# Kernel optimization log

Measured on AMD Instinct MI355X. Metric: run time of the kernel, lower is better.

Reference implementation:

```python
import jax, jax.numpy as jnp
import numpy as np

B, V, L = 2, 12000, 16
IN_F = 479  # 3+3+3+9+3+10+64+256(imgf)+128(gar_latent)


def setup_inputs() -> dict:
    key = jax.random.key(0)
    ks = jax.random.split(key, 12)

    def w(k, shape, fan_in):
        return (jax.random.normal(k, shape, jnp.float32) / np.sqrt(fan_in)).astype(jnp.float32)

    return {
        "x": jax.random.normal(ks[0], (B, V, IN_F), jnp.float32),
        "spiral_idx": jax.random.randint(ks[1], (V + 1, L), 0, V + 1),  # indices incl. dummy vertex V
        "W_point": w(ks[2], (IN_F, 256), IN_F),                 # pointMLP Linear, no bias
        "res1_W": w(ks[3], (2, 256 * L, 256), 256 * L),          # two SpiralConv(256,256)
        "res1_b": jnp.zeros((2, 256), jnp.float32),
        "W_mid": w(ks[4], (256, 128), 256),                      # midDown, no bias
        "ress_W": w(ks[5], (3, 2, 128 * L, 128), 128 * L),       # 3 residual blocks of SpiralConv(128,128)
        "ress_b": jnp.zeros((3, 2, 128), jnp.float32),
        "Wo1": w(ks[6], (512, 256), 512), "bo1": jnp.zeros((256,), jnp.float32),
        "Wo2": w(ks[7], (256, 128), 256), "bo2": jnp.zeros((128,), jnp.float32),
        "Wo3": w(ks[8], (128, 3), 128),  "bo3": jnp.zeros((3,), jnp.float32),
    }


def _spiral_conv(x, idx, Wc, bc, zp):
    # x: [B, Vp, C]; idx: [Vp, L] -> gather spiral neighborhoods then linear, mask dummy vertex
    Bn, Vp, C = x.shape
    g = x[:, idx.reshape(-1), :].reshape(Bn, Vp, -1)  # [B, Vp, L*C]
    return (g @ Wc + bc) * zp


def _res_block(x, idx, Wb, bb, zp):
    h = jax.nn.relu(_spiral_conv(x, idx, Wb[0], bb[0], zp))
    h = _spiral_conv(h, idx, Wb[1], bb[1], zp)
    return jax.nn.relu(h + x)


def reference(x, spiral_idx, W_point, res1_W, res1_b, W_mid, ress_W, ress_b,
              Wo1, bo1, Wo2, bo2, Wo3, bo3):
    pf = jax.nn.relu(x @ W_point)                                  # [B, V, 256]
    Bn = pf.shape[0]
    pfs = jnp.concatenate([pf, jnp.zeros((Bn, 1, pf.shape[-1]), pf.dtype)], axis=1)  # [B, V+1, 256]
    Vp = pfs.shape[1]
    zp = jnp.ones((1, Vp, 1), pf.dtype).at[0, -1, 0].set(0.0)       # zero_padding mask
    fs = (_res_block(pfs, spiral_idx, res1_W, res1_b, zp) @ W_mid) * zp  # [B, Vp, 128]
    gfs = jnp.max(fs[:, :-1, :], axis=1, keepdims=True)             # masked global max-pool [B,1,128]
    for i in range(3):
        fs = _res_block(fs, spiral_idx, ress_W[i], ress_b[i], zp)
    g = jnp.broadcast_to(gfs, (Bn, Vp, gfs.shape[-1])) * zp
    h = jnp.concatenate([pfs, fs, g], axis=-1)                      # [B, Vp, 512]
    h = jax.nn.relu(h @ Wo1 + bo1)
    h = jax.nn.relu(h @ Wo2 + bo2)
    out = h @ Wo3 + bo3
    return out[:, :-1, :]                                           # drop dummy vertex
```

## Files before the change

### kernel.cpp

```cpp
#include <hip/hip_runtime.h>
#include <cstdint>
#include <cfloat>
#include <cstddef>

constexpr int BATCH  = 2;
constexpr int V      = 12000;
constexpr int VP     = V + 1;
constexpr int M_ROWS = BATCH * VP;
constexpr int L_SP   = 16;

typedef _Float16 half_t;
typedef _Float16 half8 __attribute__((ext_vector_type(8)));
typedef float floatx4 __attribute__((ext_vector_type(4)));

__device__ __forceinline__ void async_cp16(const void* g, void* l) {
    __builtin_amdgcn_global_load_lds(
        (const __attribute__((address_space(1))) unsigned int*)g,
        (__attribute__((address_space(3))) unsigned int*)l, 16, 0, 0);
}

template<bool GATHER, int BM, int LGC>
__global__ __launch_bounds__(256, 4)
void gemm_mfma(const half_t* __restrict__ A, const half_t* __restrict__ Wt,
               const float* __restrict__ bias, const half_t* __restrict__ res,
               const int* __restrict__ idx, half_t* __restrict__ out,
               int M, int N, int K, int KA, int relu, int mask)
{
    constexpr int AF = BM / 32;
    __shared__ half_t As[BM * 64];
    __shared__ half_t Bs[64 * 64];

    const int tid  = threadIdx.x;
    const int lane = tid & 63;
    const int w    = tid >> 6;
    const int bm   = blockIdx.x, bn = blockIdx.y;

    const int goff = (((lane & 7) ^ ((lane >> 3) & 7)) << 3);
    const int rsub = lane >> 3;

    const int nB0 = bn * 64 + (w << 3) + rsub;
    const half_t* wp0 = Wt + (size_t)nB0 * K + goff;
    const half_t* wp1 = Wt + (size_t)(nB0 + 32) * K + goff;
    half_t* lB0 = &Bs[(size_t)((w << 6) + lane) * 8];
    half_t* lB1 = &Bs[(size_t)(((w + 4) << 6) + lane) * 8];

    int bb[AF], vv[AF];
    const half_t* aP[AF];
    half_t* lA[AF];
#pragma unroll
    for (int ai = 0; ai < AF; ++ai) {
        const int blk = w + (ai << 2);
        int m = bm * BM + (blk << 3) + rsub;
        if (m >= M) m = M - 1;
        bb[ai] = m / VP; vv[ai] = m - bb[ai] * VP;
        aP[ai] = GATHER ? nullptr : (A + (size_t)m * KA + goff);
        lA[ai] = &As[(size_t)((blk << 6) + lane) * 8];
    }

    const int wm = (w >> 1) * (BM / 2);
    const int wn = (w & 1) << 5;
    const int fr = lane & 15;
    const int q  = lane >> 4;
    const int f7 = fr & 7;

    floatx4 acc[AF][2] = {};

    int curl = -1;
    const half_t* gp[AF];
    const int Cm1 = (1 << LGC) - 1;

    const int nk = K >> 6;
    for (int t = 0; t < nk; ++t) {
        const int k0 = t << 6;
        if (GATHER) {
            const int l = k0 >> LGC;
            if (l != curl) {
                curl = l;
#pragma unroll
                for (int ai = 0; ai < AF; ++ai) {
                    const int j = idx[(vv[ai] << 4) + l];
                    gp[ai] = A + (((size_t)(bb[ai] * VP + j)) << LGC) + goff;
                }
            }
            const int ko = k0 & Cm1;
#pragma unroll
            for (int ai = 0; ai < AF; ++ai) async_cp16(gp[ai] + ko, lA[ai]);
        } else {
#pragma unroll
            for (int ai = 0; ai < AF; ++ai) async_cp16(aP[ai] + k0, lA[ai]);
        }
        async_cp16(wp0 + k0, lB0);
        async_cp16(wp1 + k0, lB1);
        __syncthreads();

#pragma unroll
        for (int s = 0; s < 2; ++s) {
            const int ck = ((((s << 2) | q) ^ f7) << 3);
            half8 af[AF], bf[2];
#pragma unroll
            for (int i = 0; i < AF; ++i)
                af[i] = *(const half8*)&As[(wm + (i << 4) + fr) * 64 + ck];
#pragma unroll
            for (int j = 0; j < 2; ++j)
                bf[j] = *(const half8*)&Bs[(wn + (j << 4) + fr) * 64 + ck];
#pragma unroll
            for (int i = 0; i < AF; ++i)
#pragma unroll
                for (int j = 0; j < 2; ++j)
                    acc[i][j] = __builtin_amdgcn_mfma_f32_16x16x32_f16(af[i], bf[j], acc[i][j], 0, 0, 0);
        }
        __syncthreads();
    }

    const int er = q << 2;
#pragma unroll
    for (int i = 0; i < AF; ++i) {
#pragma unroll
        for (int j = 0; j < 2; ++j) {
            const int n = bn * 64 + wn + (j << 4) + fr;
            const floatx4 a = acc[i][j];
#pragma unroll
            for (int r = 0; r < 4; ++r) {
                const int m = bm * BM + wm + (i << 4) + er + r;
                if (m >= M) continue;
                float val = a[r];
                if (bias) val += bias[n];
                if (res)  val += (float)res[(size_t)m * N + n];
                if (relu) val = fmaxf(val, 0.f);
                const int vvm = m - (m / VP) * VP;
                if (mask && vvm == VP - 1) val = 0.f;
                out[(size_t)m * N + n] = (half_t)val;
            }
        }
    }
}

__global__ void wcvt(const float* __restrict__ in, half_t* __restrict__ out,
                     int K, int N, int Kpad)
{
    __shared__ float t[32][33];
    const size_t ioff = (size_t)blockIdx.z * K * N;
    const size_t ooff = (size_t)blockIdx.z * N * Kpad;
    const int k0 = blockIdx.x * 32, n0 = blockIdx.y * 32;
    const int tx = threadIdx.x & 31, ty = threadIdx.x >> 5;
#pragma unroll
    for (int r = 0; r < 4; ++r) {
        const int k = k0 + ty + r * 8;
        t[ty + r * 8][tx] = (k < K && n0 + tx < N) ? in[ioff + (size_t)k * N + n0 + tx] : 0.f;
    }
    __syncthreads();
#pragma unroll
    for (int r = 0; r < 4; ++r) {
        const int n = n0 + ty + r * 8;
        const int k = k0 + tx;
        if (n < N && k < Kpad) out[ooff + (size_t)n * Kpad + k] = (half_t)t[tx][ty + r * 8];
    }
}

__global__ void cvt_x(const float* __restrict__ x, half_t* __restrict__ xh)
{
    const int m = blockIdx.x;
    const int b = m / VP, v = m - b * VP;
    for (int k = threadIdx.x; k < 512; k += 256) {
        float val = (v < V && k < 479) ? x[((size_t)b * V + v) * 479 + k] : 0.f;
        xh[(size_t)m * 512 + k] = (half_t)val;
    }
}

__global__ void maxpool1(const half_t* __restrict__ fs, float* __restrict__ pmax)
{
    const int b = blockIdx.x, chunk = blockIdx.y;
    const int c = threadIdx.x;
    const int v0 = chunk * (V / 32);
    float m = -FLT_MAX;
    const half_t* p = fs + ((size_t)b * VP + v0) * 128 + c;
    for (int v = 0; v < V / 32; ++v) { m = fmaxf(m, (float)*p); p += 128; }
    pmax[((size_t)b * 32 + chunk) * 128 + c] = m;
}
__global__ void maxpool2(const float* __restrict__ pmax, half_t* __restrict__ gfs)
{
    const int b = blockIdx.x, c = threadIdx.x;
    float m = -FLT_MAX;
    for (int i = 0; i < 32; ++i) m = fmaxf(m, pmax[((size_t)b * 32 + i) * 128 + c]);
    gfs[b * 128 + c] = (half_t)m;
}

__global__ void concat_k(const half_t* __restrict__ pfs, const half_t* __restrict__ fs,
                         const half_t* __restrict__ gfs, half_t* __restrict__ h)
{
    const size_t i = (size_t)blockIdx.x * 256 + threadIdx.x;
    if (i >= (size_t)M_ROWS * 512) return;
    const int    n   = (int)(i & 511);
    const size_t row = i >> 9;
    const int    b   = (int)(row / VP);
    const int    v   = (int)(row - (size_t)b * VP);
    half_t val;
    if (n < 256)      val = pfs[row * 256 + n];
    else if (n < 384) val = fs[row * 128 + (n - 256)];
    else              val = (v == VP - 1) ? (half_t)0.f : gfs[b * 128 + (n - 384)];
    h[i] = val;
}

__global__ void final_k(const half_t* __restrict__ h, const float* __restrict__ Wo3,
                        const float* __restrict__ bo3, float* __restrict__ out)
{
    __shared__ float wsm[384];
    __shared__ float b3[3];
    for (int t = threadIdx.x; t < 384; t += 256) wsm[t] = Wo3[t];
    if (threadIdx.x < 3) b3[threadIdx.x] = bo3[threadIdx.x];
    __syncthreads();

    const int gid = blockIdx.x * 256 + threadIdx.x;
    if (gid >= BATCH * V) return;
    const int b = gid / V;
    const int v = gid - b * V;
    const half_t* hr = h + ((size_t)b * VP + v) * 128;

    float o0 = b3[0], o1 = b3[1], o2 = b3[2];
#pragma unroll 4
    for (int c = 0; c < 128; ++c) {
        const float hv = (float)hr[c];
        o0 += hv * wsm[c * 3 + 0];
        o1 += hv * wsm[c * 3 + 1];
        o2 += hv * wsm[c * 3 + 2];
    }
    out[(size_t)gid * 3 + 0] = o0;
    out[(size_t)gid * 3 + 1] = o1;
    out[(size_t)gid * 3 + 2] = o2;
}

extern "C" void kernel_launch(void* const* d_in, const int* in_sizes, int n_in,
                              void* d_out, int out_size, void* d_ws, size_t ws_size,
                              hipStream_t stream)
{
    const float* x       = (const float*)d_in[0];
    const int*   sidx    = (const int*)  d_in[1];
    const float* W_point = (const float*)d_in[2];
    const float* res1_W  = (const float*)d_in[3];
    const float* res1_b  = (const float*)d_in[4];
    const float* W_mid   = (const float*)d_in[5];
    const float* ress_W  = (const float*)d_in[6];
    const float* ress_b  = (const float*)d_in[7];
    const float* Wo1     = (const float*)d_in[8];
    const float* bo1     = (const float*)d_in[9];
    const float* Wo2     = (const float*)d_in[10];
    const float* bo2     = (const float*)d_in[11];
    const float* Wo3     = (const float*)d_in[12];
    const float* bo3     = (const float*)d_in[13];
    float* out = (float*)d_out;

    char* p = (char*)d_ws;
    auto alloc = [&](size_t bytes) { char* q = p; p += (bytes + 255) & ~(size_t)255; return q; };
    const size_t fs_bytes = (size_t)M_ROWS * 128 * 2;
    half_t* reg0 = (half_t*)alloc((size_t)M_ROWS * 512 * 2);
    half_t* pfs  = (half_t*)alloc((size_t)M_ROWS * 256 * 2);
    char*   rA   = alloc((size_t)M_ROWS * 256 * 2);
    char*   rB   = alloc((size_t)M_ROWS * 256 * 2);
    half_t* Wpt_t  = (half_t*)alloc((size_t)256 * 512 * 2);
    half_t* r1Wt   = (half_t*)alloc((size_t)2 * 256 * 4096 * 2);
    half_t* Wmid_t = (half_t*)alloc((size_t)128 * 256 * 2);
    half_t* rsWt   = (half_t*)alloc((size_t)6 * 128 * 2048 * 2);
    half_t* Wo1_t  = (half_t*)alloc((size_t)256 * 512 * 2);
    half_t* Wo2_t  = (half_t*)alloc((size_t)128 * 256 * 2);
    float*  pmax   = (float*)alloc((size_t)2 * 32 * 128 * 4);
    half_t* gfs    = (half_t*)alloc(512);

    half_t* bufA = (half_t*)rA;
    half_t* bufB = (half_t*)rB;
    half_t* fsA  = (half_t*)rA;
    half_t* fsB  = (half_t*)(rA + fs_bytes);
    half_t* tmp  = (half_t*)rB;
    half_t* h512 = reg0;
    half_t* h256 = (half_t*)rB;
    half_t* h128 = (half_t*)rA;

    const dim3 blk(256);

    wcvt<<<dim3(16, 8, 1),  blk, 0, stream>>>(W_point, Wpt_t, 479, 256, 512);
    wcvt<<<dim3(128, 8, 2), blk, 0, stream>>>(res1_W, r1Wt, 4096, 256, 4096);
    wcvt<<<dim3(8, 4, 1),   blk, 0, stream>>>(W_mid, Wmid_t, 256, 128, 256);
    wcvt<<<dim3(64, 4, 6),  blk, 0, stream>>>(ress_W, rsWt, 2048, 128, 2048);
    wcvt<<<dim3(16, 8, 1),  blk, 0, stream>>>(Wo1, Wo1_t, 512, 256, 512);
    wcvt<<<dim3(8, 4, 1),   blk, 0, stream>>>(Wo2, Wo2_t, 256, 128, 256);
    cvt_x<<<M_ROWS, blk, 0, stream>>>(x, reg0);

    const int mg64 = (M_ROWS + 63) / 64;
    const int mg32 = (M_ROWS + 31) / 32;

    gemm_mfma<false, 64, 0><<<dim3(mg64, 4), blk, 0, stream>>>(
        reg0, Wpt_t, nullptr, nullptr, nullptr, pfs,
        M_ROWS, 256, 512, 512, 1, 1);

    gemm_mfma<true, 64, 8><<<dim3(mg64, 4), blk, 0, stream>>>(
        pfs, r1Wt, res1_b, nullptr, sidx, bufA,
        M_ROWS, 256, 4096, 0, 1, 1);

    gemm_mfma<true, 64, 8><<<dim3(mg64, 4), blk, 0, stream>>>(
        bufA, r1Wt + (size_t)256 * 4096, res1_b + 256, pfs, sidx, bufB,
        M_ROWS, 256, 4096, 0, 1, 1);

    gemm_mfma<false, 32, 0><<<dim3(mg32, 2), blk, 0, stream>>>(
        bufB, Wmid_t, nullptr, nullptr, nullptr, fsA,
        M_ROWS, 128, 256, 256, 0, 1);

    maxpool1<<<dim3(BATCH, 32), dim3(128), 0, stream>>>(fsA, pmax);
    maxpool2<<<dim3(BATCH), dim3(128), 0, stream>>>(pmax, gfs);

    half_t* cur = fsA;
    half_t* nxt = fsB;
    for (int i = 0; i < 3; ++i) {
        const half_t* Wa = rsWt + (size_t)(2 * i + 0) * 128 * 2048;
        const half_t* Wb = rsWt + (size_t)(2 * i + 1) * 128 * 2048;
        const float* ba = ress_b + (2 * i + 0) * 128;
        const float* bb = ress_b + (2 * i + 1) * 128;
        gemm_mfma<true, 32, 7><<<dim3(mg32, 2), blk, 0, stream>>>(
            cur, Wa, ba, nullptr, sidx, tmp,
            M_ROWS, 128, 2048, 0, 1, 1);
        gemm_mfma<true, 32, 7><<<dim3(mg32, 2), blk, 0, stream>>>(
            tmp, Wb, bb, cur, sidx, nxt,
            M_ROWS, 128, 2048, 0, 1, 1);
        half_t* t2 = cur; cur = nxt; nxt = t2;
    }

    concat_k<<<(unsigned)(((size_t)M_ROWS * 512 + 255) / 256), blk, 0, stream>>>(
        pfs, cur, gfs, h512);

    gemm_mfma<false, 64, 0><<<dim3(mg64, 4), blk, 0, stream>>>(
        h512, Wo1_t, bo1, nullptr, nullptr, h256,
        M_ROWS, 256, 512, 512, 1, 0);

    gemm_mfma<false, 32, 0><<<dim3(mg32, 2), blk, 0, stream>>>(
        h256, Wo2_t, bo2, nullptr, nullptr, h128,
        M_ROWS, 128, 256, 256, 1, 0);

    final_k<<<(BATCH * V + 255) / 256, blk, 0, stream>>>(h128, Wo3, bo3, out);
}
```

Baseline: 638.5 us.

## Double-buffer GEMM tiles, widen N tile to 128, and cache spiral indices in LDS

The MFMA GEMM now double-buffers its A and B shared-memory tiles, so the async global-to-LDS loads for the next K step are issued before computing the current one. This removes one barrier per iteration. The block tile grows from 64 to 128 columns, with BM doubled at every call site, so each A gather is reused across more output columns. Spiral indices are preloaded into LDS once per block. In exchange the kernel uses more LDS and more accumulator registers, occupancy drops (launch bounds go to 2-3 blocks per CU), and fewer blocks are launched.

```diff
diff --git a/kernel.cpp b/kernel.cpp
--- a/kernel.cpp
+++ b/kernel.cpp
@@ -20,15 +20,16 @@
 }
 
 template<bool GATHER, int BM, int LGC>
-__global__ __launch_bounds__(256, 4)
+__global__ __launch_bounds__(256, (BM == 128 ? 2 : 3))
 void gemm_mfma(const half_t* __restrict__ A, const half_t* __restrict__ Wt,
                const float* __restrict__ bias, const half_t* __restrict__ res,
                const int* __restrict__ idx, half_t* __restrict__ out,
                int M, int N, int K, int KA, int relu, int mask)
 {
     constexpr int AF = BM / 32;
-    __shared__ half_t As[BM * 64];
-    __shared__ half_t Bs[64 * 64];
+    __shared__ half_t As[2 * BM * 64];
+    __shared__ half_t Bs[2 * 128 * 64];
+    __shared__ int    idx_l[GATHER ? BM * 16 : 1];
 
     const int tid  = threadIdx.x;
     const int lane = tid & 63;
@@ -38,86 +39,102 @@
     const int goff = (((lane & 7) ^ ((lane >> 3) & 7)) << 3);
     const int rsub = lane >> 3;
 
-    const int nB0 = bn * 64 + (w << 3) + rsub;
-    const half_t* wp0 = Wt + (size_t)nB0 * K + goff;
-    const half_t* wp1 = Wt + (size_t)(nB0 + 32) * K + goff;
-    half_t* lB0 = &Bs[(size_t)((w << 6) + lane) * 8];
-    half_t* lB1 = &Bs[(size_t)(((w + 4) << 6) + lane) * 8];
-
-    int bb[AF], vv[AF];
+    if (GATHER) {
+        for (int e = tid; e < BM * 16; e += 256) {
+            const int r = e >> 4, l = e & 15;
+            int m = bm * BM + r; if (m >= M) m = M - 1;
+            const int v = m - (m / VP) * VP;
+            idx_l[e] = idx[(v << 4) + l];
+        }
+    }
+
+    const half_t* wp[4];
+#pragma unroll
+    for (int bi = 0; bi < 4; ++bi) {
+        const int r = ((w + (bi << 2)) << 3) + rsub;
+        wp[bi] = Wt + (size_t)(bn * 128 + r) * K + goff;
+    }
+
+    int arow[AF], abase[AF];
     const half_t* aP[AF];
-    half_t* lA[AF];
 #pragma unroll
     for (int ai = 0; ai < AF; ++ai) {
-        const int blk = w + (ai << 2);
-        int m = bm * BM + (blk << 3) + rsub;
-        if (m >= M) m = M - 1;
-        bb[ai] = m / VP; vv[ai] = m - bb[ai] * VP;
+        const int r = ((w + (ai << 2)) << 3) + rsub;
+        arow[ai] = r;
+        int m = bm * BM + r; if (m >= M) m = M - 1;
+        const int b = m / VP;
+        abase[ai] = b * VP;
         aP[ai] = GATHER ? nullptr : (A + (size_t)m * KA + goff);
-        lA[ai] = &As[(size_t)((blk << 6) + lane) * 8];
     }
 
     const int wm = (w >> 1) * (BM / 2);
-    const int wn = (w & 1) << 5;
+    const int wn = (w & 1) << 6;
     const int fr = lane & 15;
     const int q  = lane >> 4;
     const int f7 = fr & 7;
 
-    floatx4 acc[AF][2] = {};
-
-    int curl = -1;
-    const half_t* gp[AF];
-    const int Cm1 = (1 << LGC) - 1;
-
+    floatx4 acc[AF][4] = {};
+
+    auto stage = [&](int t, int bs) {
+        const int k0 = t << 6;
+        half_t* Ad = As + bs * (BM * 64);
+        half_t* Bd = Bs + bs * (128 * 64);
+        if (GATHER) {
+            const int l  = k0 >> LGC;
+            const int ko = k0 & ((1 << LGC) - 1);
+#pragma unroll
+            for (int ai = 0; ai < AF; ++ai) {
+                const int j = idx_l[(arow[ai] << 4) + l];
+                const half_t* g = A + (((size_t)(abase[ai] + j)) << LGC) + ko + goff;
+                async_cp16(g, Ad + ((w + (ai << 2)) << 9) + (lane << 3));
+            }
+        } else {
+#pragma unroll
+            for (int ai = 0; ai < AF; ++ai)
+                async_cp16(aP[ai] + k0, Ad + ((w + (ai << 2)) << 9) + (lane << 3));
+        }
+#pragma unroll
+        for (int bi = 0; bi < 4; ++bi)
+            async_cp16(wp[bi] + k0, Bd + ((w + (bi << 2)) << 9) + (lane << 3));
+    };
+
+    auto compute = [&](int bs) {
+        const half_t* Ab = As + bs * (BM * 64);
+        const half_t* Bb = Bs + bs * (128 * 64);
+#pragma unroll
+        for (int s = 0; s < 2; ++s) {
+            const int ck = ((((s << 2) | q) ^ f7) << 3);
+            half8 af[AF], bf[4];
+#pragma unroll
+            for (int i = 0; i < AF; ++i)
+                af[i] = *(const half8*)&Ab[(wm + (i << 4) + fr) * 64 + ck];
+#pragma unroll
+            for (int j = 0; j < 4; ++j)
+                bf[j] = *(const half8*)&Bb[(wn + (j << 4) + fr) * 64 + ck];
+#pragma unroll
+            for (int i = 0; i < AF; ++i)
+#pragma unroll
+                for (int j = 0; j < 4; ++j)
+                    acc[i][j] = __builtin_amdgcn_mfma_f32_16x16x32_f16(af[i], bf[j], acc[i][j], 0, 0, 0);
+        }
+    };
+
+    __syncthreads();
+    stage(0, 0);
+    __syncthreads();
     const int nk = K >> 6;
     for (int t = 0; t < nk; ++t) {
-        const int k0 = t << 6;
-        if (GATHER) {
-            const int l = k0 >> LGC;
-            if (l != curl) {
-                curl = l;
-#pragma unroll
-                for (int ai = 0; ai < AF; ++ai) {
-                    const int j = idx[(vv[ai] << 4) + l];
-                    gp[ai] = A + (((size_t)(bb[ai] * VP + j)) << LGC) + goff;
-                }
-            }
-            const int ko = k0 & Cm1;
-#pragma unroll
-            for (int ai = 0; ai < AF; ++ai) async_cp16(gp[ai] + ko, lA[ai]);
-        } else {
-#pragma unroll
-            for (int ai = 0; ai < AF; ++ai) async_cp16(aP[ai] + k0, lA[ai]);
-        }
-        async_cp16(wp0 + k0, lB0);
-        async_cp16(wp1 + k0, lB1);
+        if (t + 1 < nk) stage(t + 1, (t + 1) & 1);
+        compute(t & 1);
         __syncthreads();
-
-#pragma unroll
-        for (int s = 0; s < 2; ++s) {
-            const int ck = ((((s << 2) | q) ^ f7) << 3);
-            half8 af[AF], bf[2];
-#pragma unroll
-            for (int i = 0; i < AF; ++i)
-                af[i] = *(const half8*)&As[(wm + (i << 4) + fr) * 64 + ck];
-#pragma unroll
-            for (int j = 0; j < 2; ++j)
-                bf[j] = *(const half8*)&Bs[(wn + (j << 4) + fr) * 64 + ck];
-#pragma unroll
-            for (int i = 0; i < AF; ++i)
-#pragma unroll
-                for (int j = 0; j < 2; ++j)
-                    acc[i][j] = __builtin_amdgcn_mfma_f32_16x16x32_f16(af[i], bf[j], acc[i][j], 0, 0, 0);
-        }
-        __syncthreads();
     }
 
     const int er = q << 2;
 #pragma unroll
     for (int i = 0; i < AF; ++i) {
 #pragma unroll
-        for (int j = 0; j < 2; ++j) {
-            const int n = bn * 64 + wn + (j << 4) + fr;
+        for (int j = 0; j < 4; ++j) {
+            const int n = bn * 128 + wn + (j << 4) + fr;
             const floatx4 a = acc[i][j];
 #pragma unroll
             for (int r = 0; r < 4; ++r) {
@@ -284,22 +301,22 @@
     wcvt<<<dim3(8, 4, 1),   blk, 0, stream>>>(Wo2, Wo2_t, 256, 128, 256);
     cvt_x<<<M_ROWS, blk, 0, stream>>>(x, reg0);
 
-    const int mg64 = (M_ROWS + 63) / 64;
-    const int mg32 = (M_ROWS + 31) / 32;
-
-    gemm_mfma<false, 64, 0><<<dim3(mg64, 4), blk, 0, stream>>>(
+    const int mg128 = (M_ROWS + 127) / 128;
+    const int mg64  = (M_ROWS + 63) / 64;
+
+    gemm_mfma<false, 128, 0><<<dim3(mg128, 2), blk, 0, stream>>>(
         reg0, Wpt_t, nullptr, nullptr, nullptr, pfs,
         M_ROWS, 256, 512, 512, 1, 1);
 
-    gemm_mfma<true, 64, 8><<<dim3(mg64, 4), blk, 0, stream>>>(
+    gemm_mfma<true, 128, 8><<<dim3(mg128, 2), blk, 0, stream>>>(
         pfs, r1Wt, res1_b, nullptr, sidx, bufA,
         M_ROWS, 256, 4096, 0, 1, 1);
 
-    gemm_mfma<true, 64, 8><<<dim3(mg64, 4), blk, 0, stream>>>(
+    gemm_mfma<true, 128, 8><<<dim3(mg128, 2), blk, 0, stream>>>(
         bufA, r1Wt + (size_t)256 * 4096, res1_b + 256, pfs, sidx, bufB,
         M_ROWS, 256, 4096, 0, 1, 1);
 
-    gemm_mfma<false, 32, 0><<<dim3(mg32, 2), blk, 0, stream>>>(
+    gemm_mfma<false, 64, 0><<<dim3(mg64, 1), blk, 0, stream>>>(
         bufB, Wmid_t, nullptr, nullptr, nullptr, fsA,
         M_ROWS, 128, 256, 256, 0, 1);
 
@@ -313,10 +330,10 @@
         const half_t* Wb = rsWt + (size_t)(2 * i + 1) * 128 * 2048;
         const float* ba = ress_b + (2 * i + 0) * 128;
         const float* bb = ress_b + (2 * i + 1) * 128;
-        gemm_mfma<true, 32, 7><<<dim3(mg32, 2), blk, 0, stream>>>(
+        gemm_mfma<true, 64, 7><<<dim3(mg64, 1), blk, 0, stream>>>(
             cur, Wa, ba, nullptr, sidx, tmp,
             M_ROWS, 128, 2048, 0, 1, 1);
-        gemm_mfma<true, 32, 7><<<dim3(mg32, 2), blk, 0, stream>>>(
+        gemm_mfma<true, 64, 7><<<dim3(mg64, 1), blk, 0, stream>>>(
             tmp, Wb, bb, cur, sidx, nxt,
             M_ROWS, 128, 2048, 0, 1, 1);
         half_t* t2 = cur; cur = nxt; nxt = t2;
@@ -325,11 +342,11 @@
     concat_k<<<(unsigned)(((size_t)M_ROWS * 512 + 255) / 256), blk, 0, stream>>>(
         pfs, cur, gfs, h512);
 
-    gemm_mfma<false, 64, 0><<<dim3(mg64, 4), blk, 0, stream>>>(
+    gemm_mfma<false, 128, 0><<<dim3(mg128, 2), blk, 0, stream>>>(
         h512, Wo1_t, bo1, nullptr, nullptr, h256,
         M_ROWS, 256, 512, 512, 1, 0);
 
-    gemm_mfma<false, 32, 0><<<dim3(mg32, 2), blk, 0, stream>>>(
+    gemm_mfma<false, 64, 0><<<dim3(mg64, 1), blk, 0, stream>>>(
         h256, Wo2_t, bo2, nullptr, nullptr, h128,
         M_ROWS, 128, 256, 256, 1, 0);
 
```

After: 674.1 us. 5.6% more time.

## Double-buffer LDS tiles to overlap async loads with MFMA compute

Applied to the files above, without the earlier changes.

Doubles the A and B shared-memory tiles and restructures the K loop so the next tile's async global-to-LDS copy is issued before the current tile's MFMA work. That leaves one barrier per iteration instead of two. In the gather path the spiral index for the next neighbor is also prefetched one step ahead, keeping the index load off the critical path. The cost is twice the LDS per block, which may reduce occupancy under the 4-blocks-per-CU launch bound. It also depends on the single barrier being enough to order the async writes against the reads of the other buffer.

```diff
diff --git a/kernel.cpp b/kernel.cpp
--- a/kernel.cpp
+++ b/kernel.cpp
@@ -27,8 +27,8 @@
                int M, int N, int K, int KA, int relu, int mask)
 {
     constexpr int AF = BM / 32;
-    __shared__ half_t As[BM * 64];
-    __shared__ half_t Bs[64 * 64];
+    __shared__ half_t As[2 * BM * 64];
+    __shared__ half_t Bs[2 * 64 * 64];
 
     const int tid  = threadIdx.x;
     const int lane = tid & 63;
@@ -38,23 +38,27 @@
     const int goff = (((lane & 7) ^ ((lane >> 3) & 7)) << 3);
     const int rsub = lane >> 3;
 
-    const int nB0 = bn * 64 + (w << 3) + rsub;
-    const half_t* wp0 = Wt + (size_t)nB0 * K + goff;
-    const half_t* wp1 = Wt + (size_t)(nB0 + 32) * K + goff;
-    half_t* lB0 = &Bs[(size_t)((w << 6) + lane) * 8];
-    half_t* lB1 = &Bs[(size_t)(((w + 4) << 6) + lane) * 8];
-
-    int bb[AF], vv[AF];
+    const half_t* wp[2];
+    int dstB[2];
+#pragma unroll
+    for (int bi = 0; bi < 2; ++bi) {
+        const int blk = w + (bi << 2);
+        wp[bi]  = Wt + (size_t)(bn * 64 + (blk << 3) + rsub) * K + goff;
+        dstB[bi] = (blk << 9) + (lane << 3);
+    }
+
+    int vv[AF], abase[AF], dstA[AF];
     const half_t* aP[AF];
-    half_t* lA[AF];
 #pragma unroll
     for (int ai = 0; ai < AF; ++ai) {
         const int blk = w + (ai << 2);
         int m = bm * BM + (blk << 3) + rsub;
         if (m >= M) m = M - 1;
-        bb[ai] = m / VP; vv[ai] = m - bb[ai] * VP;
+        const int b = m / VP;
+        vv[ai] = m - b * VP;
+        abase[ai] = b * VP;
         aP[ai] = GATHER ? nullptr : (A + (size_t)m * KA + goff);
-        lA[ai] = &As[(size_t)((blk << 6) + lane) * 8];
+        dstA[ai] = (blk << 9) + (lane << 3);
     }
 
     const int wm = (w >> 1) * (BM / 2);
@@ -65,51 +69,79 @@
 
     floatx4 acc[AF][2] = {};
 
-    int curl = -1;
-    const half_t* gp[AF];
-    const int Cm1 = (1 << LGC) - 1;
-
-    const int nk = K >> 6;
-    for (int t = 0; t < nk; ++t) {
+    auto stage = [&](int t, const int* jr) {
         const int k0 = t << 6;
+        half_t* Ad = As + (t & 1) * (BM * 64);
+        half_t* Bd = Bs + (t & 1) * (64 * 64);
         if (GATHER) {
-            const int l = k0 >> LGC;
-            if (l != curl) {
-                curl = l;
-#pragma unroll
-                for (int ai = 0; ai < AF; ++ai) {
-                    const int j = idx[(vv[ai] << 4) + l];
-                    gp[ai] = A + (((size_t)(bb[ai] * VP + j)) << LGC) + goff;
-                }
-            }
-            const int ko = k0 & Cm1;
-#pragma unroll
-            for (int ai = 0; ai < AF; ++ai) async_cp16(gp[ai] + ko, lA[ai]);
+            const int ko = k0 & ((1 << LGC) - 1);
+#pragma unroll
+            for (int ai = 0; ai < AF; ++ai)
+                async_cp16(A + (((size_t)(abase[ai] + jr[ai])) << LGC) + ko + goff,
+                           Ad + dstA[ai]);
         } else {
 #pragma unroll
-            for (int ai = 0; ai < AF; ++ai) async_cp16(aP[ai] + k0, lA[ai]);
-        }
-        async_cp16(wp0 + k0, lB0);
-        async_cp16(wp1 + k0, lB1);
-        __syncthreads();
-
+            for (int ai = 0; ai < AF; ++ai)
+                async_cp16(aP[ai] + k0, Ad + dstA[ai]);
+        }
+#pragma unroll
+        for (int bi = 0; bi < 2; ++bi)
+            async_cp16(wp[bi] + k0, Bd + dstB[bi]);
+    };
+
+    auto compute = [&](int bs) {
+        const half_t* Ab = As + bs * (BM * 64);
+        const half_t* Bb = Bs + bs * (64 * 64);
 #pragma unroll
         for (int s = 0; s < 2; ++s) {
             const int ck = ((((s << 2) | q) ^ f7) << 3);
             half8 af[AF], bf[2];
 #pragma unroll
             for (int i = 0; i < AF; ++i)
-                af[i] = *(const half8*)&As[(wm + (i << 4) + fr) * 64 + ck];
+                af[i] = *(const half8*)&Ab[(wm + (i << 4) + fr) * 64 + ck];
 #pragma unroll
             for (int j = 0; j < 2; ++j)
-                bf[j] = *(const half8*)&Bs[(wn + (j << 4) + fr) * 64 + ck];
+                bf[j] = *(const half8*)&Bb[(wn + (j << 4) + fr) * 64 + ck];
 #pragma unroll
             for (int i = 0; i < AF; ++i)
 #pragma unroll
                 for (int j = 0; j < 2; ++j)
                     acc[i][j] = __builtin_amdgcn_mfma_f32_16x16x32_f16(af[i], bf[j], acc[i][j], 0, 0, 0);
         }
+    };
+
+    if (GATHER) {
+        constexpr int NI = (1 << LGC) >> 6;
+        const int L = K >> LGC;
+        int jc[AF], jn[AF];
+#pragma unroll
+        for (int ai = 0; ai < AF; ++ai) jc[ai] = idx[vv[ai] << 4];
+#pragma unroll 1
+        for (int l = 0; l < L; ++l) {
+            if (l + 1 < L) {
+#pragma unroll
+                for (int ai = 0; ai < AF; ++ai) jn[ai] = idx[(vv[ai] << 4) + l + 1];
+            }
+#pragma unroll
+            for (int kc = 0; kc < NI; ++kc) {
+                const int t = l * NI + kc;
+                stage(t, jc);
+                if (t > 0) compute((t - 1) & 1);
+                __syncthreads();
+            }
+#pragma unroll
+            for (int ai = 0; ai < AF; ++ai) jc[ai] = jn[ai];
+        }
+        compute(((K >> 6) - 1) & 1);
+    } else {
+        const int nk = K >> 6;
+        stage(0, nullptr);
         __syncthreads();
+        for (int t = 0; t < nk; ++t) {
+            if (t + 1 < nk) stage(t + 1, nullptr);
+            compute(t & 1);
+            __syncthreads();
+        }
     }
 
     const int er = q << 2;
```

After: 695.3 us. +8.9%, slower.
